# Kernel tuning notes

Hardware: AMD Instinct MI355X
Metric: run time of the kernel (lower is better)

The kernel has to match this reference:

```python
import jax, jax.numpy as jnp
import numpy as np

NUM_FREQS = 8
TEMPERATURE = 100.0
DOWNSAMPLE = 64
GRID = 8
D_OUT = 512


def fourier_embed(x):
    # x: [M, 2] -> [M, NUM_FREQS*2*2], order: per freq [sin(f*x), cos(f*x)]
    freqs = TEMPERATURE ** (jnp.arange(NUM_FREQS, dtype=jnp.float32) / NUM_FREQS)
    xf = x[:, None, :] * freqs[None, :, None]  # [M, F, 2]
    feats = jnp.stack([jnp.sin(xf), jnp.cos(xf)], axis=2)  # [M, F, 2, 2]
    return feats.reshape(x.shape[0], -1)  # [M, 32]


def mlp(x, W1, b1, W2, b2, W3, b3):
    h = jax.nn.silu(x @ W1 + b1)
    h = jax.nn.silu(h @ W2 + b2)
    return h @ W3 + b3


def scatter_to_grid(drags, emb):
    # drags: [BV, N, 2] (pixel coords), emb: [BV, N, 512]
    BV, N, _ = drags.shape
    r = drags[..., 0].astype(jnp.int32) // DOWNSAMPLE  # [BV, N]
    c = drags[..., 1].astype(jnp.int32) // DOWNSAMPLE
    idx = r * GRID + c  # flat cell index in [0, 64)
    b_idx = jnp.arange(BV)[:, None]
    grid = jnp.zeros((BV, GRID * GRID, D_OUT), emb.dtype).at[b_idx, idx].add(emb)
    # -> [BV, 512, 8, 8]
    return grid.transpose(0, 2, 1).reshape(BV, D_OUT, GRID, GRID)


def setup_inputs() -> dict:
    key = jax.random.key(0)
    ks = jax.random.split(key, 8)
    B, V, N = 8, 8, 1024
    IMG = GRID * DOWNSAMPLE  # 512
    drags_start = jax.random.uniform(ks[0], (B, V, N, 2), jnp.float32) * IMG
    drags_end = jax.random.uniform(ks[1], (B, V, N, 2), jnp.float32) * IMG
    pd = NUM_FREQS * 2 * 2  # 32
    W1 = jax.random.normal(ks[2], (pd, 128), jnp.float32) * (1.0 / np.sqrt(pd))
    b1 = jnp.zeros((128,), jnp.float32)
    W2 = jax.random.normal(ks[3], (128, 256), jnp.float32) * (1.0 / np.sqrt(128))
    b2 = jnp.zeros((256,), jnp.float32)
    W3 = jax.random.normal(ks[4], (256, 512), jnp.float32) * (1.0 / np.sqrt(256))
    b3 = jnp.zeros((512,), jnp.float32)
    return dict(drags_start=drags_start, drags_end=drags_end,
                W1=W1, b1=b1, W2=W2, b2=b2, W3=W3, b3=b3)


def reference(drags_start, drags_end, W1, b1, W2, b2, W3, b3):
    B, V, N, _ = drags_start.shape
    BV = B * V
    ds = drags_start.reshape(BV, N, 2)
    de = drags_end.reshape(BV, N, 2)

    def embed(d):  # [BV, N, 2] -> [BV, N, 512]
        feats = fourier_embed(d.reshape(BV * N, 2))  # no_grad in torch
        return mlp(feats, W1, b1, W2, b2, W3, b3).reshape(BV, N, D_OUT)

    emb_s = embed(ds)
    emb_e = embed(de)
    merge_s = scatter_to_grid(ds, emb_s)
    merge_e = scatter_to_grid(de, emb_e)
    return jnp.concatenate([merge_s, merge_e], axis=1)  # [BV, 1024, 8, 8]
```

## Files before the change

kernel.cpp:

```cpp
#include <hip/hip_runtime.h>
#include <hip/hip_bf16.h>

typedef _Float16 half8 __attribute__((ext_vector_type(8)));
typedef _Float16 half4v __attribute__((ext_vector_type(4)));
typedef float floatx4 __attribute__((ext_vector_type(4)));
typedef unsigned int uint2v __attribute__((ext_vector_type(2)));

__device__ const float FREQS[8] = {
    1.0f, 1.7782794100389228f, 3.1622776601683795f, 5.623413251903491f,
    10.0f, 17.78279410038923f, 31.622776601683793f, 56.23413251903491f};

__device__ inline void fsincos(float m, float& s, float& c) {
  constexpr double I2PI_D = 0.15915494309189533576888376337251;
  constexpr float HI = (float)I2PI_D;
  constexpr float LO = (float)(I2PI_D - (double)HI);
  float k = rintf(m * HI);
  float f = fmaf(m, HI, -k);
  f = fmaf(m, LO, f);
  s = __builtin_amdgcn_sinf(f);
  c = __builtin_amdgcn_cosf(f);
}

__device__ inline float fsilu(float x) {
  return x * __builtin_amdgcn_rcpf(1.f + __expf(-x));
}

__global__ __launch_bounds__(256) void prep_weights(
    const float* __restrict__ W1, const float* __restrict__ W2,
    const float* __restrict__ W3, _Float16* __restrict__ W1t,
    _Float16* __restrict__ W2t, _Float16* __restrict__ W3f) {
  int tid = blockIdx.x * blockDim.x + threadIdx.x;
  int stride = gridDim.x * blockDim.x;
  for (int i = tid; i < 128 * 32; i += stride) {
    int n = i >> 5, k = i & 31;
    W1t[i] = (_Float16)W1[k * 128 + n];
  }
  for (int i = tid; i < 256 * 128; i += stride) {
    int n = i >> 7, k = i & 127;
    W2t[i] = (_Float16)W2[k * 256 + n];
  }
  for (int i = tid; i < 512 * 256; i += stride) {
    int k = i >> 9, n = i & 511;
    int it = n >> 4, ln = n & 15, ks = k >> 5, q = (k >> 3) & 3, j = k & 7;
    W3f[((size_t)(it * 8 + ks) * 64 + q * 16 + ln) * 8 + j] = (_Float16)W3[i];
  }
}

#define HS 136
#define OHS 136
__global__ __launch_bounds__(512, 4) void embed_scatter(
    const float* __restrict__ dstart, const float* __restrict__ dend,
    const float* __restrict__ b1, const float* __restrict__ b2,
    const _Float16* __restrict__ W1t, const _Float16* __restrict__ W2t,
    _Float16* __restrict__ swz, int* __restrict__ counts) {
  __shared__ __align__(16) _Float16 h1t[128 * HS];
  __shared__ __align__(16) _Float16 oneh[64 * OHS];
  __shared__ __align__(16) _Float16 W1lds[4096];
  __shared__ float b1lds[128];
  __shared__ int hist[64];

  int bid = blockIdx.x;
  int bv = bid >> 3, tsel = (bid >> 2) & 1, pg = bid & 3;
  const float* src = tsel ? dend : dstart;
  int tid = threadIdx.x;
  int lane = tid & 63, w = tid >> 6, ln = lane & 15, q = lane >> 4;

  *(half8*)&W1lds[tid * 8] = *(const half8*)&W1t[tid * 8];
  if (tid < 128) b1lds[tid] = b1[tid];
  if (tid < 64) hist[tid] = 0;
  {
    half8 zz = {};
    for (int i = tid; i < (64 * OHS) / 8; i += 512) ((half8*)oneh)[i] = zz;
  }

  half8 w2f[2][4];
  float b2v[2];
  for (int nt = 0; nt < 2; nt++) {
    int n = w * 32 + nt * 16 + ln;
    b2v[nt] = b2[n];
    for (int ks = 0; ks < 4; ks++)
      w2f[nt][ks] = *(const half8*)&W2t[n * 128 + ks * 32 + q * 8];
  }
  floatx4 sacc[4][2];
  for (int mc = 0; mc < 4; mc++)
    for (int nt = 0; nt < 2; nt++) sacc[mc][nt] = (floatx4){0.f, 0.f, 0.f, 0.f};

  float fA = FREQS[2 * q], fB = FREQS[2 * q + 1];
  int pbase = bv * 1024 + pg * 256;
  __syncthreads();

  for (int c = 0; c < 2; c++) {
    if (c) {
      half8 zz = {};
      for (int i = tid; i < (64 * OHS) / 8; i += 512) ((half8*)oneh)[i] = zz;
      __syncthreads();
    }
    int pl = c * 128 + w * 16 + ln;
    float2 xy = *(const float2*)&src[(size_t)(pbase + pl) * 2];
    if (q == 0) {
      int cell = ((int)xy.x >> 6) * 8 + ((int)xy.y >> 6);
      atomicAdd(&hist[cell], 1);
      oneh[cell * OHS + w * 16 + ln] = (_Float16)1.0f;
    }
    half8 fb;
    {
      float s, cc2;
      fsincos(xy.x * fA, s, cc2); fb[0] = (_Float16)s; fb[2] = (_Float16)cc2;
      fsincos(xy.y * fA, s, cc2); fb[1] = (_Float16)s; fb[3] = (_Float16)cc2;
      fsincos(xy.x * fB, s, cc2); fb[4] = (_Float16)s; fb[6] = (_Float16)cc2;
      fsincos(xy.y * fB, s, cc2); fb[5] = (_Float16)s; fb[7] = (_Float16)cc2;
    }
#pragma unroll 2
    for (int mtW = 0; mtW < 8; mtW++) {
      half8 w1f = *(const half8*)&W1lds[(mtW * 16 + ln) * 32 + q * 8];
      floatx4 c1 = *(const floatx4*)&b1lds[mtW * 16 + q * 4];
      c1 = __builtin_amdgcn_mfma_f32_16x16x32_f16(w1f, fb, c1, 0, 0, 0);
      half4v hv;
      for (int r = 0; r < 4; r++) hv[r] = (_Float16)fsilu(c1[r]);
      *(half4v*)&h1t[(w * 16 + ln) * HS + mtW * 16 + q * 4] = hv;
    }
    __syncthreads();
#pragma unroll 1
    for (int mt = 0; mt < 8; mt++) {
      half8 af[4];
      for (int ks = 0; ks < 4; ks++)
        af[ks] = *(const half8*)&h1t[(mt * 16 + ln) * HS + ks * 32 + q * 8];
      floatx4 cc0 = {b2v[0], b2v[0], b2v[0], b2v[0]};
      floatx4 cc1 = {b2v[1], b2v[1], b2v[1], b2v[1]};
      for (int ks = 0; ks < 4; ks++) {
        cc0 = __builtin_amdgcn_mfma_f32_16x16x32_f16(af[ks], w2f[0][ks], cc0, 0, 0, 0);
        cc1 = __builtin_amdgcn_mfma_f32_16x16x32_f16(af[ks], w2f[1][ks], cc1, 0, 0, 0);
      }
      half4v hb0, hb1;
      for (int r = 0; r < 4; r++) {
        hb0[r] = (_Float16)fsilu(cc0[r]);
        hb1[r] = (_Float16)fsilu(cc1[r]);
      }
      for (int mc = 0; mc < 4; mc++) {
        half4v ao = *(const half4v*)&oneh[(mc * 16 + ln) * OHS + mt * 16 + q * 4];
        sacc[mc][0] = __builtin_amdgcn_mfma_f32_16x16x16f16(ao, hb0, sacc[mc][0], 0, 0, 0);
        sacc[mc][1] = __builtin_amdgcn_mfma_f32_16x16x16f16(ao, hb1, sacc[mc][1], 0, 0, 0);
      }
    }
    __syncthreads();
  }
  for (int mc = 0; mc < 4; mc++)
    for (int nt = 0; nt < 2; nt++) {
      half4v hv;
      for (int r = 0; r < 4; r++) hv[r] = (_Float16)sacc[mc][nt][r];
      *(half4v*)&swz[((((size_t)bid * 4 + mc) * 16 + w * 2 + nt) * 64 + lane) * 4] = hv;
    }
  if (tid < 64) counts[bid * 64 + tid] = hist[tid];
}

#define AS 264
__global__ __launch_bounds__(256) void layer3(
    const _Float16* __restrict__ swz, const int* __restrict__ counts,
    const _Float16* __restrict__ W3f, const float* __restrict__ b3,
    float* __restrict__ out) {
  __shared__ _Float16 a_lds[16 * AS];
  __shared__ float cnt_s[16];
  int bb = blockIdx.x;
  int bvts = bb >> 2, cq = bb & 3;
  int tid = threadIdx.x;
  for (int it = 0; it < 4; it++) {
    int cc = it * 256 + tid;
    int wn = cc >> 6, lane2 = cc & 63, q2 = lane2 >> 4, ln2 = lane2 & 15;
    size_t base = ((size_t)bvts * 16 + cq) * 1024 + cc;
    half4v s = (*(const half4v*)&swz[base * 4] +
                *(const half4v*)&swz[(base + 4096) * 4]) +
               (*(const half4v*)&swz[(base + 8192) * 4] +
                *(const half4v*)&swz[(base + 12288) * 4]);
    int col = wn * 16 + ln2;
    for (int r = 0; r < 4; r++) a_lds[(q2 * 4 + r) * AS + col] = s[r];
  }
  if (tid < 16) {
    int base = bvts * 4 * 64 + cq * 16 + tid;
    cnt_s[tid] = (float)(counts[base] + counts[base + 64] +
                         counts[base + 128] + counts[base + 192]);
  }
  __syncthreads();
  int lane = tid & 63, w = tid >> 6, ln = lane & 15, q = lane >> 4;
  half8 af[8];
  for (int ks = 0; ks < 8; ks++)
    af[ks] = *(const half8*)&a_lds[ln * AS + ks * 32 + q * 8];
  float cntf = cnt_s[ln];
  for (int ii = 0; ii < 8; ii++) {
    int i = w * 8 + ii;
    half8 wf[8];
    for (int ks = 0; ks < 8; ks++)
      wf[ks] = *(const half8*)&W3f[((size_t)(i * 8 + ks) * 64 + lane) * 8];
    floatx4 b3v = *(const floatx4*)&b3[i * 16 + q * 4];
    floatx4 acc = {0.f, 0.f, 0.f, 0.f};
    for (int ks = 0; ks < 8; ks++)
      acc = __builtin_amdgcn_mfma_f32_16x16x32_f16(wf[ks], af[ks], acc, 0, 0, 0);
    for (int r = 0; r < 4; r++)
      out[((size_t)bvts * 512 + i * 16 + q * 4 + r) * 64 + cq * 16 + ln] =
          acc[r] + cntf * b3v[r];
  }
}

extern "C" void kernel_launch(void* const* d_in, const int* in_sizes, int n_in,
                              void* d_out, int out_size, void* d_ws, size_t ws_size,
                              hipStream_t stream) {
  const float* dstart = (const float*)d_in[0];
  const float* dend = (const float*)d_in[1];
  const float* W1 = (const float*)d_in[2];
  const float* b1 = (const float*)d_in[3];
  const float* W2 = (const float*)d_in[4];
  const float* b2 = (const float*)d_in[5];
  const float* W3 = (const float*)d_in[6];
  const float* b3 = (const float*)d_in[7];
  float* out = (float*)d_out;

  char* ws = (char*)d_ws;
  _Float16* W1t = (_Float16*)(ws);
  _Float16* W2t = (_Float16*)(ws + 8192);
  _Float16* W3f = (_Float16*)(ws + 73728);
  _Float16* swz = (_Float16*)(ws + 335872);
  int* counts = (int*)(ws + 335872 + 16777216);

  hipLaunchKernelGGL(prep_weights, dim3(64), dim3(256), 0, stream,
                     W1, W2, W3, W1t, W2t, W3f);
  hipLaunchKernelGGL(embed_scatter, dim3(512), dim3(512), 0, stream,
                     dstart, dend, b1, b2, W1t, W2t, swz, counts);
  hipLaunchKernelGGL(layer3, dim3(512), dim3(256), 0, stream,
                     swz, counts, W3f, b3, out);
}
```

Measured before the change: 115.1 us.

## Fold W1/W2 conversion into embed kernel, vectorize W3 prep, widen layer3 tiles

```diff
diff --git a/kernel.cpp b/kernel.cpp
--- a/kernel.cpp
+++ b/kernel.cpp
@@ -4,7 +4,7 @@
 typedef _Float16 half8 __attribute__((ext_vector_type(8)));
 typedef _Float16 half4v __attribute__((ext_vector_type(4)));
 typedef float floatx4 __attribute__((ext_vector_type(4)));
-typedef unsigned int uint2v __attribute__((ext_vector_type(2)));
+typedef float float4v __attribute__((ext_vector_type(4)));
 
 __device__ const float FREQS[8] = {
     1.0f, 1.7782794100389228f, 3.1622776601683795f, 5.623413251903491f,
@@ -25,33 +25,23 @@
   return x * __builtin_amdgcn_rcpf(1.f + __expf(-x));
 }
 
-__global__ __launch_bounds__(256) void prep_weights(
-    const float* __restrict__ W1, const float* __restrict__ W2,
-    const float* __restrict__ W3, _Float16* __restrict__ W1t,
-    _Float16* __restrict__ W2t, _Float16* __restrict__ W3f) {
-  int tid = blockIdx.x * blockDim.x + threadIdx.x;
-  int stride = gridDim.x * blockDim.x;
-  for (int i = tid; i < 128 * 32; i += stride) {
-    int n = i >> 5, k = i & 31;
-    W1t[i] = (_Float16)W1[k * 128 + n];
-  }
-  for (int i = tid; i < 256 * 128; i += stride) {
-    int n = i >> 7, k = i & 127;
-    W2t[i] = (_Float16)W2[k * 256 + n];
-  }
-  for (int i = tid; i < 512 * 256; i += stride) {
-    int k = i >> 9, n = i & 511;
-    int it = n >> 4, ln = n & 15, ks = k >> 5, q = (k >> 3) & 3, j = k & 7;
-    W3f[((size_t)(it * 8 + ks) * 64 + q * 16 + ln) * 8 + j] = (_Float16)W3[i];
-  }
+__global__ __launch_bounds__(256) void prep_w3(
+    const float* __restrict__ W3, _Float16* __restrict__ W3f) {
+  int f = blockIdx.x * 256 + threadIdx.x;
+  int ln = f & 15, q = (f >> 4) & 3, ks = (f >> 6) & 7, it = f >> 9;
+  int n = it * 16 + ln;
+  half8 t;
+  for (int j = 0; j < 8; j++)
+    t[j] = (_Float16)W3[(size_t)(ks * 32 + q * 8 + j) * 512 + n];
+  *(half8*)&W3f[(size_t)f * 8] = t;
 }
 
 #define HS 136
 #define OHS 136
 __global__ __launch_bounds__(512, 4) void embed_scatter(
     const float* __restrict__ dstart, const float* __restrict__ dend,
-    const float* __restrict__ b1, const float* __restrict__ b2,
-    const _Float16* __restrict__ W1t, const _Float16* __restrict__ W2t,
+    const float* __restrict__ W1, const float* __restrict__ b1,
+    const float* __restrict__ W2, const float* __restrict__ b2,
     _Float16* __restrict__ swz, int* __restrict__ counts) {
   __shared__ __align__(16) _Float16 h1t[128 * HS];
   __shared__ __align__(16) _Float16 oneh[64 * OHS];
@@ -65,7 +55,15 @@
   int tid = threadIdx.x;
   int lane = tid & 63, w = tid >> 6, ln = lane & 15, q = lane >> 4;
 
-  *(half8*)&W1lds[tid * 8] = *(const half8*)&W1t[tid * 8];
+  {
+    float4v v0 = *(const float4v*)&W1[tid * 8];
+    float4v v1 = *(const float4v*)&W1[tid * 8 + 4];
+    for (int e = 0; e < 8; e++) {
+      int idx = tid * 8 + e;
+      int k = idx >> 7, n = idx & 127;
+      W1lds[n * 32 + k] = (_Float16)(e < 4 ? v0[e] : v1[e - 4]);
+    }
+  }
   if (tid < 128) b1lds[tid] = b1[tid];
   if (tid < 64) hist[tid] = 0;
   {
@@ -78,8 +76,12 @@
   for (int nt = 0; nt < 2; nt++) {
     int n = w * 32 + nt * 16 + ln;
     b2v[nt] = b2[n];
-    for (int ks = 0; ks < 4; ks++)
-      w2f[nt][ks] = *(const half8*)&W2t[n * 128 + ks * 32 + q * 8];
+    for (int ks = 0; ks < 4; ks++) {
+      half8 t;
+      for (int j = 0; j < 8; j++)
+        t[j] = (_Float16)W2[(size_t)(ks * 32 + q * 8 + j) * 256 + n];
+      w2f[nt][ks] = t;
+    }
   }
   floatx4 sacc[4][2];
   for (int mc = 0; mc < 4; mc++)
@@ -87,18 +89,16 @@
 
   float fA = FREQS[2 * q], fB = FREQS[2 * q + 1];
   int pbase = bv * 1024 + pg * 256;
+  int prevcell = 0;
   __syncthreads();
 
   for (int c = 0; c < 2; c++) {
-    if (c) {
-      half8 zz = {};
-      for (int i = tid; i < (64 * OHS) / 8; i += 512) ((half8*)oneh)[i] = zz;
-      __syncthreads();
-    }
     int pl = c * 128 + w * 16 + ln;
     float2 xy = *(const float2*)&src[(size_t)(pbase + pl) * 2];
     if (q == 0) {
       int cell = ((int)xy.x >> 6) * 8 + ((int)xy.y >> 6);
+      if (c) oneh[prevcell * OHS + w * 16 + ln] = (_Float16)0.0f;
+      prevcell = cell;
       atomicAdd(&hist[cell], 1);
       oneh[cell * OHS + w * 16 + ln] = (_Float16)1.0f;
     }
@@ -158,45 +158,48 @@
     const _Float16* __restrict__ swz, const int* __restrict__ counts,
     const _Float16* __restrict__ W3f, const float* __restrict__ b3,
     float* __restrict__ out) {
-  __shared__ _Float16 a_lds[16 * AS];
-  __shared__ float cnt_s[16];
+  __shared__ _Float16 a_lds[64 * AS];
+  __shared__ float cnt_s[64];
   int bb = blockIdx.x;
-  int bvts = bb >> 2, cq = bb & 3;
+  int bvts = bb >> 1, oh = bb & 1;
   int tid = threadIdx.x;
-  for (int it = 0; it < 4; it++) {
-    int cc = it * 256 + tid;
-    int wn = cc >> 6, lane2 = cc & 63, q2 = lane2 >> 4, ln2 = lane2 & 15;
-    size_t base = ((size_t)bvts * 16 + cq) * 1024 + cc;
+  for (int it = 0; it < 16; it++) {
+    int f = it * 256 + tid;
+    size_t base = ((size_t)bvts * 4) * 4096 + f;
     half4v s = (*(const half4v*)&swz[base * 4] +
                 *(const half4v*)&swz[(base + 4096) * 4]) +
                (*(const half4v*)&swz[(base + 8192) * 4] +
                 *(const half4v*)&swz[(base + 12288) * 4]);
-    int col = wn * 16 + ln2;
-    for (int r = 0; r < 4; r++) a_lds[(q2 * 4 + r) * AS + col] = s[r];
-  }
-  if (tid < 16) {
-    int base = bvts * 4 * 64 + cq * 16 + tid;
+    int mc = f >> 10, wnt = (f >> 6) & 15, lane2 = f & 63;
+    int q2 = lane2 >> 4, ln2 = lane2 & 15;
+    int k = wnt * 16 + ln2;
+    for (int r = 0; r < 4; r++) a_lds[(mc * 16 + q2 * 4 + r) * AS + k] = s[r];
+  }
+  if (tid < 64) {
+    int base = bvts * 4 * 64 + tid;
     cnt_s[tid] = (float)(counts[base] + counts[base + 64] +
                          counts[base + 128] + counts[base + 192]);
   }
   __syncthreads();
   int lane = tid & 63, w = tid >> 6, ln = lane & 15, q = lane >> 4;
-  half8 af[8];
-  for (int ks = 0; ks < 8; ks++)
-    af[ks] = *(const half8*)&a_lds[ln * AS + ks * 32 + q * 8];
-  float cntf = cnt_s[ln];
-  for (int ii = 0; ii < 8; ii++) {
-    int i = w * 8 + ii;
+  for (int ii = 0; ii < 4; ii++) {
+    int ig = oh * 16 + w * 4 + ii;
     half8 wf[8];
     for (int ks = 0; ks < 8; ks++)
-      wf[ks] = *(const half8*)&W3f[((size_t)(i * 8 + ks) * 64 + lane) * 8];
-    floatx4 b3v = *(const floatx4*)&b3[i * 16 + q * 4];
-    floatx4 acc = {0.f, 0.f, 0.f, 0.f};
-    for (int ks = 0; ks < 8; ks++)
-      acc = __builtin_amdgcn_mfma_f32_16x16x32_f16(wf[ks], af[ks], acc, 0, 0, 0);
-    for (int r = 0; r < 4; r++)
-      out[((size_t)bvts * 512 + i * 16 + q * 4 + r) * 64 + cq * 16 + ln] =
-          acc[r] + cntf * b3v[r];
+      wf[ks] = *(const half8*)&W3f[((size_t)(ig * 8 + ks) * 64 + lane) * 8];
+    floatx4 b3v = *(const floatx4*)&b3[ig * 16 + q * 4];
+    for (int ct = 0; ct < 4; ct++) {
+      half8 af[8];
+      for (int ks = 0; ks < 8; ks++)
+        af[ks] = *(const half8*)&a_lds[(ct * 16 + ln) * AS + ks * 32 + q * 8];
+      floatx4 acc = {0.f, 0.f, 0.f, 0.f};
+      for (int ks = 0; ks < 8; ks++)
+        acc = __builtin_amdgcn_mfma_f32_16x16x32_f16(wf[ks], af[ks], acc, 0, 0, 0);
+      float cntf = cnt_s[ct * 16 + ln];
+      for (int r = 0; r < 4; r++)
+        out[((size_t)bvts * 512 + ig * 16 + q * 4 + r) * 64 + ct * 16 + ln] =
+            acc[r] + cntf * b3v[r];
+    }
   }
 }
 
@@ -214,16 +217,13 @@
   float* out = (float*)d_out;
 
   char* ws = (char*)d_ws;
-  _Float16* W1t = (_Float16*)(ws);
-  _Float16* W2t = (_Float16*)(ws + 8192);
-  _Float16* W3f = (_Float16*)(ws + 73728);
-  _Float16* swz = (_Float16*)(ws + 335872);
-  int* counts = (int*)(ws + 335872 + 16777216);
-
-  hipLaunchKernelGGL(prep_weights, dim3(64), dim3(256), 0, stream,
-                     W1, W2, W3, W1t, W2t, W3f);
+  _Float16* W3f = (_Float16*)(ws);
+  _Float16* swz = (_Float16*)(ws + 262144);
+  int* counts = (int*)(ws + 262144 + 16777216);
+
+  hipLaunchKernelGGL(prep_w3, dim3(64), dim3(256), 0, stream, W3, W3f);
   hipLaunchKernelGGL(embed_scatter, dim3(512), dim3(512), 0, stream,
-                     dstart, dend, b1, b2, W1t, W2t, swz, counts);
-  hipLaunchKernelGGL(layer3, dim3(512), dim3(256), 0, stream,
+                     dstart, dend, W1, b1, W2, b2, swz, counts);
+  hipLaunchKernelGGL(layer3, dim3(256), dim3(256), 0, stream,
                      swz, counts, W3f, b3, out);
 }
```

Result: faster. 111.5 us (-3.1%).
